# Kernel optimization log

Hardware: AMD Instinct MI355X
Metric: run time of the kernel (lower is better)

## Reference

```python
import jax, jax.numpy as jnp
import numpy as np

# --- 5G LDPC BG1-structured code parameters (k=8000, n=16000, r=0.5) ---
Z = 384          # lifting factor
KB = 22          # info-bit base columns (BG1)
MB = 46          # base rows (BG1)
NB = 68          # base columns (BG1)
K = 8000         # info bits per codeword
N = 16000        # rate-matched codeword bits
BATCH = 2048
K_LDPC = KB * Z  # 8448
N_LDPC = NB * Z  # 26112
M_A = 4 * Z      # rows of A / size of B (core parity block)
M_C = (MB - 4) * Z  # 16128 remaining parity bits
NBPS = 4         # bits per QAM symbol (16-QAM interleaver)


def _lift(base_rows, base_cols, shifts):
    """Expand base-graph entries into lifted circulant (row, col) index lists."""
    br = np.asarray(base_rows, np.int64)
    bc = np.asarray(base_cols, np.int64)
    sh = np.asarray(shifts, np.int64)
    r = np.arange(Z, dtype=np.int64)
    rows = (br[:, None] * Z + r[None, :]).ravel()
    cols = (bc[:, None] * Z + (r[None, :] + sh[:, None]) % Z).ravel()
    order = np.argsort(rows, kind='stable')
    return rows[order].astype(np.int32), cols[order].astype(np.int32)


def _build_code_indices():
    rng = np.random.RandomState(0)
    mask = rng.rand(4, KB) < 0.35
    mask[:, 0] = True  # guarantee non-empty rows
    ar, ac = np.nonzero(mask)
    a_rows, a_cols = _lift(ar, ac, rng.randint(0, Z, size=ar.size))
    # B_inv: GF(2) inverse of lower-bidiagonal identity-block B ->
    # block lower-triangular of identity circulants (shift 0)
    br = [i for i in range(4) for j in range(i + 1)]
    bc = [j for i in range(4) for j in range(i + 1)]
    bi_rows, bi_cols = _lift(br, bc, np.zeros(len(br), np.int64))
    # C1: base rows 4..45 (local 0..41) x info cols 0..21
    mask = rng.rand(MB - 4, KB) < 0.15
    mask[:, 1] = True
    c1r, c1c = np.nonzero(mask)
    c1_rows, c1_cols = _lift(c1r, c1c, rng.randint(0, Z, size=c1r.size))
    # C2: base rows 4..45 (local) x core-parity cols 22..25 (local 0..3)
    mask = rng.rand(MB - 4, 4) < 0.35
    mask[:, 0] = True
    c2r, c2c = np.nonzero(mask)
    c2_rows, c2_cols = _lift(c2r, c2c, rng.randint(0, Z, size=c2r.size))
    # Output interleaver (Sec. 5.4.2.2): perm[i + j*m] = i*(n/m) + j
    out_int = np.arange(N, dtype=np.int32).reshape(NBPS, N // NBPS).T.ravel()
    return a_rows, a_cols, bi_rows, bi_cols, c1_rows, c1_cols, c2_rows, c2_cols, out_int


def setup_inputs() -> dict:
    key = jax.random.key(0)
    u = jax.random.randint(key, (BATCH, K), 0, 2).astype(jnp.float32)
    (a_rows, a_cols, bi_rows, bi_cols,
     c1_rows, c1_cols, c2_rows, c2_cols, out_int) = _build_code_indices()
    return {
        'u': u,
        'a_rows': jnp.asarray(a_rows), 'a_cols': jnp.asarray(a_cols),
        'bi_rows': jnp.asarray(bi_rows), 'bi_cols': jnp.asarray(bi_cols),
        'c1_rows': jnp.asarray(c1_rows), 'c1_cols': jnp.asarray(c1_cols),
        'c2_rows': jnp.asarray(c2_rows), 'c2_cols': jnp.asarray(c2_cols),
        'out_int': jnp.asarray(out_int),
    }


def _gf2_matmul(rows, cols, xT, m):
    """Sparse GF(2) matmul via gather + segment-sum + mod 2. xT: [dim_in, B]."""
    return jnp.mod(jax.ops.segment_sum(xT[cols], rows, num_segments=m), 2.0)


def reference(u, a_rows, a_cols, bi_rows, bi_cols,
              c1_rows, c1_cols, c2_rows, c2_cols, out_int):
    B = u.shape[0]
    # shortening: append k_ldpc - k filler zeros
    uT = jnp.concatenate([u, jnp.zeros((B, K_LDPC - K), u.dtype)], axis=1).T  # [k_ldpc, B]
    # core parity: p_a = B^-1 (A u)  over GF(2)
    auT = _gf2_matmul(a_rows, a_cols, uT, M_A)        # [4z, B]
    paT = _gf2_matmul(bi_rows, bi_cols, auT, M_A)     # [4z, B]
    # extension parity: p_b = C1 u + C2 p_a  over GF(2)
    s = (jax.ops.segment_sum(uT[c1_cols], c1_rows, num_segments=M_C)
         + jax.ops.segment_sum(paT[c2_cols], c2_rows, num_segments=M_C))
    pbT = jnp.mod(s, 2.0)                             # [42z, B]
    cT = jnp.concatenate([uT, paT, pbT], axis=0)      # [n_ldpc, B]
    # remove filler bits, puncture first 2z bits, take n bits
    c_nf = jnp.concatenate([cT[:K], cT[K_LDPC:]], axis=0)
    c_short = jax.lax.dynamic_slice_in_dim(c_nf, 2 * Z, N, axis=0)  # [n, B]
    # rate-matching output interleaver
    return c_short[out_int].T                          # [B, n]
```

## Files before the change

### kernel.cpp

```cpp
#include <hip/hip_runtime.h>
#include <stdint.h>

#define Zc      384
#define K_INFO  8000
#define N_OUT   16000
#define K_LDPC  8448
#define M_A     1536
#define PB_USED 7232
#define WPR     64
#define BATCH   2048


__device__ __forceinline__ int lb(const int* __restrict__ a, int n, int key) {
  int lo = 0, hi = n;
  while (lo < hi) {
    int mid = (lo + hi) >> 1;
    if (a[mid] < key) lo = mid + 1; else hi = mid;
  }
  return lo;
}

__global__ __launch_bounds__(256) void k_pack(const float* __restrict__ u,
                                              uint32_t* __restrict__ u_pack,
                                              uint32_t* __restrict__ uT) {
  __shared__ float tile[64][65];
  __shared__ uint64_t bw[64];
  const int k0 = blockIdx.x * 64;
  const int b0 = blockIdx.y * 64;
  const int tid = threadIdx.x;

  #pragma unroll
  for (int i = 0; i < 16; ++i) {
    int lin = tid + i * 256;
    int bb = lin >> 6, kk = lin & 63;
    int k = k0 + kk;
    float v = 0.0f;
    if (k < K_INFO) v = u[(size_t)(b0 + bb) * K_INFO + k];
    tile[bb][kk] = v;
  }
  __syncthreads();

  const int lane = tid & 63;
  const int wv   = tid >> 6;
  #pragma unroll
  for (int kk = 0; kk < 16; ++kk) {
    int kp = wv * 16 + kk;
    uint64_t m = __ballot(tile[lane][kp] != 0.0f);
    if (lane == 0) bw[kp] = m;
  }
  __syncthreads();

  if (tid < 64) {
    int row = k0 + tid;
    ((uint64_t*)(u_pack + (size_t)row * WPR))[blockIdx.y] = bw[tid];
  }
  if (tid < 128) {
    int half = tid >> 6, kk = tid & 63;
    uT[(size_t)(2 * blockIdx.y + half) * K_LDPC + k0 + kk] =
        (uint32_t)(bw[kk] >> (32 * half));
  }
}

__global__ __launch_bounds__(256) void k_gf2(const int* __restrict__ rows,
                                             const int* __restrict__ cols, int nnz,
                                             const uint32_t* __restrict__ src,
                                             uint32_t* __restrict__ dst,
                                             uint32_t* __restrict__ dstT, int mT,
                                             int m) {
  const int r = blockIdx.x * 4 + (threadIdx.x >> 6);
  const int lane = threadIdx.x & 63;
  if (r >= m) return;
  const int lo = lb(rows, nnz, r);
  const int hi = lb(rows, nnz, r + 1);
  uint32_t acc = 0;
  for (int e = lo; e < hi; ++e)
    acc ^= src[(size_t)cols[e] * WPR + lane];
  dst[(size_t)r * WPR + lane] = acc;
  if (dstT) dstT[(size_t)lane * mT + r] = acc;
}

__global__ __launch_bounds__(256) void k_ext(const int* __restrict__ c1_rows,
                                             const int* __restrict__ c1_cols, int nc1,
                                             const int* __restrict__ c2_rows,
                                             const int* __restrict__ c2_cols, int nc2,
                                             const uint32_t* __restrict__ u_pack,
                                             const uint32_t* __restrict__ pa,
                                             uint32_t* __restrict__ pbT) {
  const int r = blockIdx.x * 4 + (threadIdx.x >> 6);
  const int lane = threadIdx.x & 63;
  if (r >= PB_USED) return;

  uint32_t acc = 0;
  int lo = lb(c1_rows, nc1, r), hi = lb(c1_rows, nc1, r + 1);
  for (int e = lo; e < hi; ++e)
    acc ^= u_pack[(size_t)c1_cols[e] * WPR + lane];
  lo = lb(c2_rows, nc2, r); hi = lb(c2_rows, nc2, r + 1);
  for (int e = lo; e < hi; ++e)
    acc ^= pa[(size_t)c2_cols[e] * WPR + lane];

  pbT[(size_t)lane * PB_USED + r] = acc;
}

__global__ __launch_bounds__(256) void k_out(const uint32_t* __restrict__ uT,
                                             const uint32_t* __restrict__ paT,
                                             const uint32_t* __restrict__ pbT,
                                             const int* __restrict__ out_int,
                                             float* __restrict__ out) {
  const int t = blockIdx.x * 256 + threadIdx.x;
  if (t >= N_OUT / 4) return;
  const int b = blockIdx.y;
  const int w = b >> 5, bit = b & 31;

  const uint32_t* bu = uT  + (size_t)w * K_LDPC;
  const uint32_t* bp = paT + (size_t)w * M_A;
  const uint32_t* bq = pbT + (size_t)w * PB_USED;

  const int4 oi = *(const int4*)(out_int + 4 * t);

  float o[4];
  int rr[4] = {oi.x, oi.y, oi.z, oi.w};
  #pragma unroll
  for (int j = 0; j < 4; ++j) {
    int row = 768 + rr[j];
    uint32_t wv;
    if (row < 8000)       wv = bu[row];
    else if (row < 9536)  wv = bp[row - 8000];
    else                  wv = bq[row - 9536];
    o[j] = (float)((wv >> bit) & 1u);
  }
  float4 v = {o[0], o[1], o[2], o[3]};
  *(float4*)(out + (size_t)b * N_OUT + 4 * t) = v;
}

extern "C" void kernel_launch(void* const* d_in, const int* in_sizes, int n_in,
                              void* d_out, int out_size, void* d_ws, size_t ws_size,
                              hipStream_t stream) {
  const float* u      = (const float*)d_in[0];
  const int* a_rows   = (const int*)d_in[1];
  const int* a_cols   = (const int*)d_in[2];
  const int* bi_rows  = (const int*)d_in[3];
  const int* bi_cols  = (const int*)d_in[4];
  const int* c1_rows  = (const int*)d_in[5];
  const int* c1_cols  = (const int*)d_in[6];
  const int* c2_rows  = (const int*)d_in[7];
  const int* c2_cols  = (const int*)d_in[8];
  const int* out_int  = (const int*)d_in[9];
  const int na  = in_sizes[1];
  const int nbi = in_sizes[3];
  const int nc1 = in_sizes[5];
  const int nc2 = in_sizes[7];

  char* ws = (char*)d_ws;
  uint32_t* u_pack = (uint32_t*)(ws + 0);
  uint32_t* uT     = (uint32_t*)(ws + 2162688);
  uint32_t* au     = (uint32_t*)(ws + 4325376);
  uint32_t* pa     = (uint32_t*)(ws + 4718592);
  uint32_t* paT    = (uint32_t*)(ws + 5111808);
  uint32_t* pbT    = (uint32_t*)(ws + 5505024);
  float* out = (float*)d_out;

  k_pack<<<dim3(K_LDPC / 64, BATCH / 64), 256, 0, stream>>>(u, u_pack, uT);
  k_gf2<<<dim3(M_A / 4), 256, 0, stream>>>(a_rows, a_cols, na, u_pack,
                                           au, (uint32_t*)nullptr, 0, M_A);
  k_gf2<<<dim3(M_A / 4), 256, 0, stream>>>(bi_rows, bi_cols, nbi, au,
                                           pa, paT, M_A, M_A);
  k_ext<<<dim3(PB_USED / 4), 256, 0, stream>>>(c1_rows, c1_cols, nc1,
                                               c2_rows, c2_cols, nc2,
                                               u_pack, pa, pbT);
  k_out<<<dim3((N_OUT / 4 + 255) / 256, BATCH), 256, 0, stream>>>(uT, paT, pbT,
                                                                  out_int, out);
}
```

Before: 247.5 us.

## Precompute CSR row pointers, fuse core parity kernels, widen pack loads and output writes

Adds a kernel that builds CSR row pointers once, so the per-row binary searches go away. The A and B^-1 GF(2) products are fused into one kernel that recomputes A rows on the fly, which drops the intermediate au buffer and one launch. k_pack now uses vectorised nontemporal float4 loads. k_out loads each packed word once and writes all 32 batch rows from it with nontemporal stores, cutting redundant gathers. The trade-offs are redundant recomputation of A rows inside the fused kernel and an extra launch for the row-pointer kernel.

```diff
diff --git a/kernel.cpp b/kernel.cpp
--- a/kernel.cpp
+++ b/kernel.cpp
@@ -10,6 +10,18 @@
 #define WPR     64
 #define BATCH   2048
 
+typedef float f4v __attribute__((ext_vector_type(4)));
+typedef unsigned int u32;
+
+#define OFF_UPACK 0
+#define OFF_UT    2162688
+#define OFF_PA    4325376
+#define OFF_PAT   4718592
+#define OFF_PBT   5111808
+#define OFF_RPA   6963200
+#define OFF_RPBI  6969600
+#define OFF_RPC1  6976000
+#define OFF_RPC2  7005184
 
 __device__ __forceinline__ int lb(const int* __restrict__ a, int n, int key) {
   int lo = 0, hi = n;
@@ -20,9 +32,21 @@
   return lo;
 }
 
+__global__ __launch_bounds__(256) void k_rowptr(
+    const int* __restrict__ a_rows, int na,
+    const int* __restrict__ bi_rows, int nbi,
+    const int* __restrict__ c1_rows, int nc1,
+    const int* __restrict__ c2_rows, int nc2,
+    int* __restrict__ rp_a, int* __restrict__ rp_bi,
+    int* __restrict__ rp_c1, int* __restrict__ rp_c2) {
+  const int i = blockIdx.x * 256 + threadIdx.x;
+  if (i <= M_A)     { rp_a[i]  = lb(a_rows,  na,  i); rp_bi[i] = lb(bi_rows, nbi, i); }
+  if (i <= PB_USED) { rp_c1[i] = lb(c1_rows, nc1, i); rp_c2[i] = lb(c2_rows, nc2, i); }
+}
+
 __global__ __launch_bounds__(256) void k_pack(const float* __restrict__ u,
-                                              uint32_t* __restrict__ u_pack,
-                                              uint32_t* __restrict__ uT) {
+                                              u32* __restrict__ u_pack,
+                                              u32* __restrict__ uT) {
   __shared__ float tile[64][65];
   __shared__ uint64_t bw[64];
   const int k0 = blockIdx.x * 64;
@@ -30,13 +54,16 @@
   const int tid = threadIdx.x;
 
   #pragma unroll
-  for (int i = 0; i < 16; ++i) {
-    int lin = tid + i * 256;
-    int bb = lin >> 6, kk = lin & 63;
-    int k = k0 + kk;
-    float v = 0.0f;
-    if (k < K_INFO) v = u[(size_t)(b0 + bb) * K_INFO + k];
-    tile[bb][kk] = v;
+  for (int i = 0; i < 4; ++i) {
+    int idx = tid + i * 256;
+    int bb = idx >> 4, f4i = idx & 15;
+    int k = k0 + f4i * 4;
+    f4v v = (f4v)0.0f;
+    if (k + 3 < K_INFO)
+      v = __builtin_nontemporal_load(
+            (const f4v*)(u + (size_t)(b0 + bb) * K_INFO + k));
+    tile[bb][f4i*4+0] = v.x; tile[bb][f4i*4+1] = v.y;
+    tile[bb][f4i*4+2] = v.z; tile[bb][f4i*4+3] = v.w;
   }
   __syncthreads();
 
@@ -57,79 +84,78 @@
   if (tid < 128) {
     int half = tid >> 6, kk = tid & 63;
     uT[(size_t)(2 * blockIdx.y + half) * K_LDPC + k0 + kk] =
-        (uint32_t)(bw[kk] >> (32 * half));
-  }
-}
-
-__global__ __launch_bounds__(256) void k_gf2(const int* __restrict__ rows,
-                                             const int* __restrict__ cols, int nnz,
-                                             const uint32_t* __restrict__ src,
-                                             uint32_t* __restrict__ dst,
-                                             uint32_t* __restrict__ dstT, int mT,
-                                             int m) {
+        (u32)(bw[kk] >> (32 * half));
+  }
+}
+
+__global__ __launch_bounds__(256) void k_core(
+    const int* __restrict__ a_cols,  const int* __restrict__ rp_a,
+    const int* __restrict__ bi_cols, const int* __restrict__ rp_bi,
+    const u32* __restrict__ u_pack,
+    u32* __restrict__ pa, u32* __restrict__ paT) {
   const int r = blockIdx.x * 4 + (threadIdx.x >> 6);
   const int lane = threadIdx.x & 63;
-  if (r >= m) return;
-  const int lo = lb(rows, nnz, r);
-  const int hi = lb(rows, nnz, r + 1);
-  uint32_t acc = 0;
-  for (int e = lo; e < hi; ++e)
-    acc ^= src[(size_t)cols[e] * WPR + lane];
-  dst[(size_t)r * WPR + lane] = acc;
-  if (dstT) dstT[(size_t)lane * mT + r] = acc;
-}
-
-__global__ __launch_bounds__(256) void k_ext(const int* __restrict__ c1_rows,
-                                             const int* __restrict__ c1_cols, int nc1,
-                                             const int* __restrict__ c2_rows,
-                                             const int* __restrict__ c2_cols, int nc2,
-                                             const uint32_t* __restrict__ u_pack,
-                                             const uint32_t* __restrict__ pa,
-                                             uint32_t* __restrict__ pbT) {
+  u32 acc = 0;
+  const int lo = rp_bi[r], hi = rp_bi[r + 1];
+  for (int e = lo; e < hi; ++e) {
+    const int j = bi_cols[e];
+    const int lo2 = rp_a[j], hi2 = rp_a[j + 1];
+    for (int e2 = lo2; e2 < hi2; ++e2)
+      acc ^= u_pack[(size_t)a_cols[e2] * WPR + lane];
+  }
+  pa[(size_t)r * WPR + lane] = acc;
+  paT[(size_t)lane * M_A + r] = acc;
+}
+
+__global__ __launch_bounds__(256) void k_ext(
+    const int* __restrict__ c1_cols, const int* __restrict__ rp_c1,
+    const int* __restrict__ c2_cols, const int* __restrict__ rp_c2,
+    const u32* __restrict__ u_pack, const u32* __restrict__ pa,
+    u32* __restrict__ pbT) {
   const int r = blockIdx.x * 4 + (threadIdx.x >> 6);
   const int lane = threadIdx.x & 63;
-  if (r >= PB_USED) return;
-
-  uint32_t acc = 0;
-  int lo = lb(c1_rows, nc1, r), hi = lb(c1_rows, nc1, r + 1);
+  u32 acc = 0;
+  int lo = rp_c1[r], hi = rp_c1[r + 1];
   for (int e = lo; e < hi; ++e)
     acc ^= u_pack[(size_t)c1_cols[e] * WPR + lane];
-  lo = lb(c2_rows, nc2, r); hi = lb(c2_rows, nc2, r + 1);
+  lo = rp_c2[r]; hi = rp_c2[r + 1];
   for (int e = lo; e < hi; ++e)
     acc ^= pa[(size_t)c2_cols[e] * WPR + lane];
-
   pbT[(size_t)lane * PB_USED + r] = acc;
 }
 
-__global__ __launch_bounds__(256) void k_out(const uint32_t* __restrict__ uT,
-                                             const uint32_t* __restrict__ paT,
-                                             const uint32_t* __restrict__ pbT,
+__global__ __launch_bounds__(256) void k_out(const u32* __restrict__ uT,
+                                             const u32* __restrict__ paT,
+                                             const u32* __restrict__ pbT,
                                              const int* __restrict__ out_int,
                                              float* __restrict__ out) {
   const int t = blockIdx.x * 256 + threadIdx.x;
   if (t >= N_OUT / 4) return;
-  const int b = blockIdx.y;
-  const int w = b >> 5, bit = b & 31;
-
-  const uint32_t* bu = uT  + (size_t)w * K_LDPC;
-  const uint32_t* bp = paT + (size_t)w * M_A;
-  const uint32_t* bq = pbT + (size_t)w * PB_USED;
+  const int w = blockIdx.y;
 
   const int4 oi = *(const int4*)(out_int + 4 * t);
-
-  float o[4];
-  int rr[4] = {oi.x, oi.y, oi.z, oi.w};
+  const int rr[4] = {oi.x + 768, oi.y + 768, oi.z + 768, oi.w + 768};
+  u32 wd[4];
   #pragma unroll
   for (int j = 0; j < 4; ++j) {
-    int row = 768 + rr[j];
-    uint32_t wv;
-    if (row < 8000)       wv = bu[row];
-    else if (row < 9536)  wv = bp[row - 8000];
-    else                  wv = bq[row - 9536];
-    o[j] = (float)((wv >> bit) & 1u);
-  }
-  float4 v = {o[0], o[1], o[2], o[3]};
-  *(float4*)(out + (size_t)b * N_OUT + 4 * t) = v;
+    const int row = rr[j];
+    u32 v;
+    if (row < 8000)      v = uT [(size_t)w * K_LDPC  + row];
+    else if (row < 9536) v = paT[(size_t)w * M_A     + row - 8000];
+    else                 v = pbT[(size_t)w * PB_USED + row - 9536];
+    wd[j] = v;
+  }
+
+  float* op = out + (size_t)(w * 32) * N_OUT + 4 * t;
+  #pragma unroll
+  for (int bit = 0; bit < 32; ++bit) {
+    f4v o;
+    o.x = (float)((wd[0] >> bit) & 1u);
+    o.y = (float)((wd[1] >> bit) & 1u);
+    o.z = (float)((wd[2] >> bit) & 1u);
+    o.w = (float)((wd[3] >> bit) & 1u);
+    __builtin_nontemporal_store(o, (f4v*)(op + (size_t)bit * N_OUT));
+  }
 }
 
 extern "C" void kernel_launch(void* const* d_in, const int* in_sizes, int n_in,
@@ -151,22 +177,25 @@
   const int nc2 = in_sizes[7];
 
   char* ws = (char*)d_ws;
-  uint32_t* u_pack = (uint32_t*)(ws + 0);
-  uint32_t* uT     = (uint32_t*)(ws + 2162688);
-  uint32_t* au     = (uint32_t*)(ws + 4325376);
-  uint32_t* pa     = (uint32_t*)(ws + 4718592);
-  uint32_t* paT    = (uint32_t*)(ws + 5111808);
-  uint32_t* pbT    = (uint32_t*)(ws + 5505024);
+  u32* u_pack = (u32*)(ws + OFF_UPACK);
+  u32* uT     = (u32*)(ws + OFF_UT);
+  u32* pa     = (u32*)(ws + OFF_PA);
+  u32* paT    = (u32*)(ws + OFF_PAT);
+  u32* pbT    = (u32*)(ws + OFF_PBT);
+  int* rp_a   = (int*)(ws + OFF_RPA);
+  int* rp_bi  = (int*)(ws + OFF_RPBI);
+  int* rp_c1  = (int*)(ws + OFF_RPC1);
+  int* rp_c2  = (int*)(ws + OFF_RPC2);
   float* out = (float*)d_out;
 
+  k_rowptr<<<dim3((PB_USED + 256) / 256), 256, 0, stream>>>(
+      a_rows, na, bi_rows, nbi, c1_rows, nc1, c2_rows, nc2,
+      rp_a, rp_bi, rp_c1, rp_c2);
   k_pack<<<dim3(K_LDPC / 64, BATCH / 64), 256, 0, stream>>>(u, u_pack, uT);
-  k_gf2<<<dim3(M_A / 4), 256, 0, stream>>>(a_rows, a_cols, na, u_pack,
-                                           au, (uint32_t*)nullptr, 0, M_A);
-  k_gf2<<<dim3(M_A / 4), 256, 0, stream>>>(bi_rows, bi_cols, nbi, au,
-                                           pa, paT, M_A, M_A);
-  k_ext<<<dim3(PB_USED / 4), 256, 0, stream>>>(c1_rows, c1_cols, nc1,
-                                               c2_rows, c2_cols, nc2,
+  k_core<<<dim3(M_A / 4), 256, 0, stream>>>(a_cols, rp_a, bi_cols, rp_bi,
+                                            u_pack, pa, paT);
+  k_ext<<<dim3(PB_USED / 4), 256, 0, stream>>>(c1_cols, rp_c1, c2_cols, rp_c2,
                                                u_pack, pa, pbT);
-  k_out<<<dim3((N_OUT / 4 + 255) / 256, BATCH), 256, 0, stream>>>(uT, paT, pbT,
-                                                                  out_int, out);
-}
+  k_out<<<dim3((N_OUT / 4 + 255) / 256, WPR), 256, 0, stream>>>(uT, paT, pbT,
+                                                                out_int, out);
+}
```

Result: faster. 235.6 us (-4.8%).
